# Kernel optimization log

Measured on AMD Instinct MI355X. Metric: run time of the kernel, lower is better.

## Reference

```python
import jax, jax.numpy as jnp
import numpy as np

N = 50000       # nodes
E = 800000      # edges (before self-loops)
IN_DIM = 128
HID = 64
HEADS = 4
C = HID // HEADS  # 16 per-head channels
NEG_SLOPE = 0.2   # PyG GATConv default
BN_EPS = 1e-5


def setup_inputs() -> dict:
    key = jax.random.key(0)
    ks = jax.random.split(key, 16)
    inp = {
        "x": jax.random.normal(ks[0], (N, IN_DIM), jnp.float32),
        "edge_index": jax.random.randint(ks[1], (2, E), 0, N, dtype=jnp.int32),
    }
    def glorot(k, shape):
        fan = sum(shape)
        return jax.random.normal(k, shape, jnp.float32) * jnp.sqrt(2.0 / fan)
    # layer 0: in=IN_DIM, layer 1: in=HID
    inp["W0"] = glorot(ks[2], (IN_DIM, HEADS * C))
    inp["a_src0"] = glorot(ks[3], (HEADS, C))
    inp["a_dst0"] = glorot(ks[4], (HEADS, C))
    inp["b0"] = jnp.zeros((HEADS * C,), jnp.float32)
    inp["g0"] = jnp.ones((HID,), jnp.float32)
    inp["be0"] = jnp.zeros((HID,), jnp.float32)
    inp["W1"] = glorot(ks[5], (HID, HEADS * C))
    inp["a_src1"] = glorot(ks[6], (HEADS, C))
    inp["a_dst1"] = glorot(ks[7], (HEADS, C))
    inp["b1"] = jnp.zeros((HEADS * C,), jnp.float32)
    inp["g1"] = jnp.ones((HID,), jnp.float32)
    inp["be1"] = jnp.zeros((HID,), jnp.float32)
    return inp


def _segment_softmax(e, dst, n):
    # softmax over edges grouped by destination node, per head. e: [Et, H]
    m = jax.ops.segment_max(e, dst, num_segments=n)          # [N, H]
    ex = jnp.exp(e - m[dst])
    s = jax.ops.segment_sum(ex, dst, num_segments=n)         # [N, H]
    return ex / (s[dst] + 1e-16)


def _gat_conv(h, src, dst, W, a_s, a_d, b):
    n = h.shape[0]
    hp = (h @ W).reshape(n, HEADS, C)                        # [N, H, C]
    al_s = jnp.einsum('nhc,hc->nh', hp, a_s)                 # [N, H]
    al_d = jnp.einsum('nhc,hc->nh', hp, a_d)
    e = jax.nn.leaky_relu(al_s[src] + al_d[dst], NEG_SLOPE)  # [Et, H]
    alpha = _segment_softmax(e, dst, n)
    msg = hp[src] * alpha[:, :, None]                        # [Et, H, C]
    out = jax.ops.segment_sum(msg, dst, num_segments=n)      # [N, H, C]
    return out.reshape(n, HEADS * C) + b


def _batch_norm(h, g, b):
    mu = h.mean(axis=0)
    var = h.var(axis=0)
    return (h - mu) * jax.lax.rsqrt(var + BN_EPS) * g + b


def reference(x, edge_index, W0, a_src0, a_dst0, b0, g0, be0,
              W1, a_src1, a_dst1, b1, g1, be1):
    n = x.shape[0]
    loops = jnp.arange(n, dtype=edge_index.dtype)
    src = jnp.concatenate([edge_index[0], loops])  # PyG adds self-loops
    dst = jnp.concatenate([edge_index[1], loops])
    h = _gat_conv(x, src, dst, W0, a_src0, a_dst0, b0)
    h = _batch_norm(h, g0, be0)
    h = jax.nn.relu(h)  # dropout: identity (eval / deterministic)
    h = _gat_conv(h, src, dst, W1, a_src1, a_dst1, b1)
    h = _batch_norm(h, g1, be1)
    return h
```

## Files before the change

kernel.cpp:

```cpp
#include <hip/hip_runtime.h>
#include <hip/hip_fp16.h>

#define CAP 128

template<int K, bool APPLY_BN>
__global__ void __launch_bounds__(256, 4)
gemm_tiled(const float* __restrict__ X, const float* __restrict__ W,
           const float* __restrict__ a_s, const float* __restrict__ a_d,
           const float* __restrict__ bnsum, const float* __restrict__ bnsq,
           const float* __restrict__ g, const float* __restrict__ be,
           __half* __restrict__ hp, float* __restrict__ al_s,
           float* __restrict__ al_d, int n)
{
  __shared__ float Wl[(K / 4) * 64 * 4];
  __shared__ float Xt[64 * K];

  for (int gi = threadIdx.x; gi < (K / 4) * 64; gi += 256) {
    int k4 = gi >> 6, ln = gi & 63;
    float4 w;
    w.x = W[(k4 * 4 + 0) * 64 + ln];
    w.y = W[(k4 * 4 + 1) * 64 + ln];
    w.z = W[(k4 * 4 + 2) * 64 + ln];
    w.w = W[(k4 * 4 + 3) * 64 + ln];
    *(float4*)&Wl[gi * 4] = w;
  }

  int row0 = blockIdx.x * 64;
  int nrows = min(64, n - row0);
  float4 sc, sh;
  if (APPLY_BN) {
    int cg = (threadIdx.x & 15) * 4;
    float inv_n = 1.f / (float)n;
#pragma unroll
    for (int q = 0; q < 4; ++q) {
      float mu  = bnsum[cg + q] * inv_n;
      float var = bnsq[cg + q] * inv_n - mu * mu;
      float s   = g[cg + q] * rsqrtf(var + 1e-5f);
      ((float*)&sc)[q] = s;
      ((float*)&sh)[q] = be[cg + q] - mu * s;
    }
  }
  const float4* src = (const float4*)(X + (size_t)row0 * K);
  int nf4 = nrows * (K / 4);
  for (int i = threadIdx.x; i < nf4; i += 256) {
    float4 v = src[i];
    if (APPLY_BN) {
      v.x = fmaxf(v.x * sc.x + sh.x, 0.f);
      v.y = fmaxf(v.y * sc.y + sh.y, 0.f);
      v.z = fmaxf(v.z * sc.z + sh.z, 0.f);
      v.w = fmaxf(v.w * sc.w + sh.w, 0.f);
    }
    *(float4*)&Xt[i * 4] = v;
  }
  __syncthreads();

  int lane = threadIdx.x & 63;
  int wid  = threadIdx.x >> 6;
  int rbase = wid * 16;
  float acc[16];
#pragma unroll
  for (int r = 0; r < 16; ++r) acc[r] = 0.f;

  for (int k4 = 0; k4 < K / 4; ++k4) {
    float4 wv = *(const float4*)&Wl[(k4 * 64 + lane) * 4];
#pragma unroll
    for (int r = 0; r < 16; ++r) {
      float4 xv = *(const float4*)&Xt[(rbase + r) * K + k4 * 4];
      acc[r] += xv.x * wv.x + xv.y * wv.y + xv.z * wv.z + xv.w * wv.w;
    }
  }

  float as_l = a_s[lane], ad_l = a_d[lane];
  int h = lane >> 4, c = lane & 15;
#pragma unroll
  for (int r = 0; r < 16; ++r) {
    int lr = rbase + r;
    if (lr >= nrows) break;
    int row = row0 + lr;
    float a = acc[r];
    hp[(size_t)row * 64 + lane] = __float2half(a);
    float vs = a * as_l;
    float vd = a * ad_l;
#pragma unroll
    for (int off = 8; off >= 1; off >>= 1) {
      vs += __shfl_xor(vs, off, 64);
      vd += __shfl_xor(vd, off, 64);
    }
    if (c == 0) { al_s[row * 4 + h] = vs; al_d[row * 4 + h] = vd; }
  }
}

__global__ void hist_k(const int* __restrict__ ei, int E, int N, int* __restrict__ count)
{
  int e = blockIdx.x * 256 + threadIdx.x;
  int Et = E + N;
  if (e >= Et) return;
  int d = (e < E) ? ei[E + e] : (e - E);
  atomicAdd(&count[d], 1);
}

__global__ void scan_block_k(const int* __restrict__ count, int* __restrict__ row_ptr,
                             int* __restrict__ partial, int n)
{
  __shared__ int woff[16];
  int tid = threadIdx.x;
  int i = blockIdx.x * 1024 + tid;
  int v = (i < n) ? count[i] : 0;
  int lane = tid & 63, wid = tid >> 6;
  int incl = v;
#pragma unroll
  for (int off = 1; off < 64; off <<= 1) {
    int t = __shfl_up(incl, off, 64);
    if (lane >= off) incl += t;
  }
  if (lane == 63) woff[wid] = incl;
  __syncthreads();
  if (tid < 16) {
    int wv = woff[tid];
    int winc = wv;
#pragma unroll
    for (int off = 1; off < 16; off <<= 1) {
      int t = __shfl_up(winc, off, 64);
      if (tid >= off) winc += t;
    }
    woff[tid] = winc - wv;
    if (tid == 15) partial[blockIdx.x] = winc;
  }
  __syncthreads();
  if (i < n) row_ptr[i] = woff[wid] + incl - v;
}

__global__ void scan_partial_k(int* __restrict__ partial, int* __restrict__ row_ptr,
                               int nb, int n)
{
  int tid = threadIdx.x;
  int v = (tid < nb) ? partial[tid] : 0;
  int incl = v;
#pragma unroll
  for (int off = 1; off < 64; off <<= 1) {
    int t = __shfl_up(incl, off, 64);
    if (tid >= off) incl += t;
  }
  if (tid < nb) partial[tid] = incl - v;
  if (tid == 63) row_ptr[n] = incl;
}

__global__ void scan_add_k(int* __restrict__ row_ptr, int* __restrict__ cursor,
                           const int* __restrict__ partial, int n)
{
  int i = blockIdx.x * 1024 + threadIdx.x;
  if (i < n) {
    int r = row_ptr[i] + partial[blockIdx.x];
    row_ptr[i] = r;
    cursor[i] = r;
  }
}

__global__ void scatter_k(const int* __restrict__ ei, int E, int N,
                          int* __restrict__ cursor, int* __restrict__ col_src)
{
  int e = blockIdx.x * 256 + threadIdx.x;
  int Et = E + N;
  if (e >= Et) return;
  int s, d;
  if (e < E) { s = ei[e]; d = ei[E + e]; } else { s = d = e - E; }
  int pos = atomicAdd(&cursor[d], 1);
  col_src[pos] = s;
}

__global__ void __launch_bounds__(256)
node_agg(const int* __restrict__ row_ptr, const int* __restrict__ col_src,
         const __half* __restrict__ hp, const float* __restrict__ al_s,
         const float* __restrict__ al_d, const float* __restrict__ bias,
         float* __restrict__ hpre, float* __restrict__ bnsum, float* __restrict__ bnsq,
         int n)
{
  __shared__ float sh_ex[4][CAP * 4];
  __shared__ int   sh_s[4][CAP];
  __shared__ float shs[64], shq[64];

  int lane = threadIdx.x & 63;
  int wid  = threadIdx.x >> 6;
  int h    = lane >> 4;
  float b  = bias[lane];
  float lsum = 0.f, lsq = 0.f;
  int nwaves = gridDim.x * 4;

  for (int d = blockIdx.x * 4 + wid; d < n; d += nwaves) {
    int beg = row_ptr[d], end = row_ptr[d + 1];
    int deg = end - beg;
    const float4 ald4 = *(const float4*)(al_d + (size_t)d * 4);
    float outv;

    if (deg <= CAP) {
      float sx = 0.f, sy = 0.f, sz = 0.f, sw = 0.f;
      for (int jb = 0; jb < deg; jb += 64) {
        int jj = jb + lane;
        if (jj < deg) {
          int s = col_src[beg + jj];
          float4 as4 = *(const float4*)(al_s + (size_t)s * 4);
          float ex = as4.x + ald4.x; ex = ex >= 0.f ? ex : 0.2f * ex;
          float ey = as4.y + ald4.y; ey = ey >= 0.f ? ey : 0.2f * ey;
          float ez = as4.z + ald4.z; ez = ez >= 0.f ? ez : 0.2f * ez;
          float ew = as4.w + ald4.w; ew = ew >= 0.f ? ew : 0.2f * ew;
          ex = __expf(ex); ey = __expf(ey); ez = __expf(ez); ew = __expf(ew);
          sh_s[wid][jj] = s;
          *(float4*)&sh_ex[wid][jj * 4] = make_float4(ex, ey, ez, ew);
          sx += ex; sy += ey; sz += ez; sw += ew;
        }
      }
#pragma unroll
      for (int off = 32; off >= 1; off >>= 1) {
        sx += __shfl_xor(sx, off, 64);
        sy += __shfl_xor(sy, off, 64);
        sz += __shfl_xor(sz, off, 64);
        sw += __shfl_xor(sw, off, 64);
      }
      float denom = (h == 0) ? sx : (h == 1) ? sy : (h == 2) ? sz : sw;
      float acc = 0.f;
      int jj = 0;
      for (; jj + 8 <= deg; jj += 8) {
        int s0 = sh_s[wid][jj],     s1 = sh_s[wid][jj + 1];
        int s2 = sh_s[wid][jj + 2], s3 = sh_s[wid][jj + 3];
        int s4 = sh_s[wid][jj + 4], s5 = sh_s[wid][jj + 5];
        int s6 = sh_s[wid][jj + 6], s7 = sh_s[wid][jj + 7];
        float e0 = sh_ex[wid][(jj + 0) * 4 + h], e1 = sh_ex[wid][(jj + 1) * 4 + h];
        float e2 = sh_ex[wid][(jj + 2) * 4 + h], e3 = sh_ex[wid][(jj + 3) * 4 + h];
        float e4 = sh_ex[wid][(jj + 4) * 4 + h], e5 = sh_ex[wid][(jj + 5) * 4 + h];
        float e6 = sh_ex[wid][(jj + 6) * 4 + h], e7 = sh_ex[wid][(jj + 7) * 4 + h];
        acc += e0 * __half2float(hp[(size_t)s0 * 64 + lane]);
        acc += e1 * __half2float(hp[(size_t)s1 * 64 + lane]);
        acc += e2 * __half2float(hp[(size_t)s2 * 64 + lane]);
        acc += e3 * __half2float(hp[(size_t)s3 * 64 + lane]);
        acc += e4 * __half2float(hp[(size_t)s4 * 64 + lane]);
        acc += e5 * __half2float(hp[(size_t)s5 * 64 + lane]);
        acc += e6 * __half2float(hp[(size_t)s6 * 64 + lane]);
        acc += e7 * __half2float(hp[(size_t)s7 * 64 + lane]);
      }
      for (; jj + 4 <= deg; jj += 4) {
        int s0 = sh_s[wid][jj],     s1 = sh_s[wid][jj + 1];
        int s2 = sh_s[wid][jj + 2], s3 = sh_s[wid][jj + 3];
        float e0 = sh_ex[wid][(jj + 0) * 4 + h], e1 = sh_ex[wid][(jj + 1) * 4 + h];
        float e2 = sh_ex[wid][(jj + 2) * 4 + h], e3 = sh_ex[wid][(jj + 3) * 4 + h];
        acc += e0 * __half2float(hp[(size_t)s0 * 64 + lane]);
        acc += e1 * __half2float(hp[(size_t)s1 * 64 + lane]);
        acc += e2 * __half2float(hp[(size_t)s2 * 64 + lane]);
        acc += e3 * __half2float(hp[(size_t)s3 * 64 + lane]);
      }
      for (; jj < deg; ++jj)
        acc += sh_ex[wid][jj * 4 + h] * __half2float(hp[(size_t)sh_s[wid][jj] * 64 + lane]);
      outv = acc / (denom + 1e-16f) + b;
    } else {
      float ald_h = (h == 0) ? ald4.x : (h == 1) ? ald4.y : (h == 2) ? ald4.z : ald4.w;
      float sum = 0.f;
      for (int j = beg; j < end; ++j) {
        int s = col_src[j];
        float v = al_s[s * 4 + h] + ald_h;
        v = (v >= 0.f) ? v : 0.2f * v;
        sum += __expf(v);
      }
      float acc = 0.f;
      for (int j = beg; j < end; ++j) {
        int s = col_src[j];
        float v = al_s[s * 4 + h] + ald_h;
        v = (v >= 0.f) ? v : 0.2f * v;
        acc += __expf(v) * __half2float(hp[(size_t)s * 64 + lane]);
      }
      outv = acc / (sum + 1e-16f) + b;
    }
    hpre[(size_t)d * 64 + lane] = outv;
    lsum += outv; lsq += outv * outv;
  }

  if (threadIdx.x < 64) { shs[threadIdx.x] = 0.f; shq[threadIdx.x] = 0.f; }
  __syncthreads();
  atomicAdd(&shs[lane], lsum);
  atomicAdd(&shq[lane], lsq);
  __syncthreads();
  if (threadIdx.x < 64) {
    atomicAdd(&bnsum[threadIdx.x], shs[threadIdx.x]);
    atomicAdd(&bnsq[threadIdx.x],  shq[threadIdx.x]);
  }
}

__global__ void bn_apply(const float* __restrict__ hpre, const float* __restrict__ bnsum,
                         const float* __restrict__ bnsq, const float* __restrict__ g,
                         const float* __restrict__ be, float* __restrict__ out, int n)
{
  size_t i = (size_t)blockIdx.x * 256 + threadIdx.x;
  size_t total = (size_t)n * 64;
  if (i >= total) return;
  int c = (int)(i & 63);
  float inv_n = 1.f / (float)n;
  float mu  = bnsum[c] * inv_n;
  float var = bnsq[c] * inv_n - mu * mu;
  out[i] = (hpre[i] - mu) * rsqrtf(var + 1e-5f) * g[c] + be[c];
}

extern "C" void kernel_launch(void* const* d_in, const int* in_sizes, int n_in,
                              void* d_out, int out_size, void* d_ws, size_t ws_size,
                              hipStream_t stream) {
  const float* x   = (const float*)d_in[0];
  const int*   ei  = (const int*)d_in[1];
  const float* W0  = (const float*)d_in[2];
  const float* as0 = (const float*)d_in[3];
  const float* ad0 = (const float*)d_in[4];
  const float* b0  = (const float*)d_in[5];
  const float* g0  = (const float*)d_in[6];
  const float* be0 = (const float*)d_in[7];
  const float* W1  = (const float*)d_in[8];
  const float* as1 = (const float*)d_in[9];
  const float* ad1 = (const float*)d_in[10];
  const float* b1  = (const float*)d_in[11];
  const float* g1  = (const float*)d_in[12];
  const float* be1 = (const float*)d_in[13];
  float* out = (float*)d_out;

  int N = in_sizes[0] / 128;
  int E = in_sizes[1] / 2;
  int Et = E + N;

  char* w = (char*)d_ws;
  auto alloc = [&](size_t bytes) {
    char* p = w; w += (bytes + 255) & ~255ull; return p;
  };
  __half* hp    = (__half*)alloc((size_t)N * 64 * 2);
  float*  hpre0 = (float*)alloc((size_t)N * 64 * 4);
  float*  hpre1 = (float*)alloc((size_t)N * 64 * 4);
  float*  als   = (float*)alloc((size_t)N * 4 * 4);
  float*  ald   = (float*)alloc((size_t)N * 4 * 4);
  int*    count = (int*)alloc((size_t)N * 4);
  int*    rowp  = (int*)alloc((size_t)(N + 1) * 4);
  int*    cursor= (int*)alloc((size_t)N * 4);
  int*    parts = (int*)alloc(64 * 4);
  int*    csrc  = (int*)alloc((size_t)Et * 4);
  float*  bnsum = (float*)alloc(64 * 4);
  float*  bnsq  = (float*)alloc(64 * 4);

  dim3 blk(256);
  int gEt   = (Et + 255) / 256;
  int gN64  = (N * 64 + 255) / 256;
  int nb    = (N + 1023) / 1024;
  int gTile = (N + 63) / 64;

  hipMemsetAsync(count, 0, (size_t)N * 4, stream);
  hist_k<<<gEt, blk, 0, stream>>>(ei, E, N, count);
  scan_block_k<<<nb, 1024, 0, stream>>>(count, rowp, parts, N);
  scan_partial_k<<<1, 64, 0, stream>>>(parts, rowp, nb, N);
  scan_add_k<<<nb, 1024, 0, stream>>>(rowp, cursor, parts, N);
  scatter_k<<<gEt, blk, 0, stream>>>(ei, E, N, cursor, csrc);

  hipMemsetAsync(bnsum, 0, 64 * 4, stream);
  hipMemsetAsync(bnsq,  0, 64 * 4, stream);
  gemm_tiled<128, false><<<gTile, blk, 0, stream>>>(x, W0, as0, ad0,
                                                    nullptr, nullptr, nullptr, nullptr,
                                                    hp, als, ald, N);
  node_agg<<<2048, blk, 0, stream>>>(rowp, csrc, hp, als, ald, b0,
                                     hpre0, bnsum, bnsq, N);

  gemm_tiled<64, true><<<gTile, blk, 0, stream>>>(hpre0, W1, as1, ad1,
                                                  bnsum, bnsq, g0, be0,
                                                  hp, als, ald, N);
  hipMemsetAsync(bnsum, 0, 64 * 4, stream);
  hipMemsetAsync(bnsq,  0, 64 * 4, stream);
  node_agg<<<2048, blk, 0, stream>>>(rowp, csrc, hp, als, ald, b1,
                                     hpre1, bnsum, bnsq, N);
  bn_apply<<<gN64, blk, 0, stream>>>(hpre1, bnsum, bnsq, g1, be1, out, N);
}
```

Baseline: 329.7 us.

## Precompute edge attention weights and aggregate two destination nodes per wavefront

Adds a per-edge kernel that computes exp(leaky_relu) attention weights in CSR order, storing them as float4 alongside a new col_dst array. node_agg then reads these precomputed weights and processes two consecutive destination nodes per wavefront, so low-degree nodes use more of the 64 lanes during the gather. It also merges the memsets for the batch-norm accumulators into the count memset and writes the second layer straight into the output buffer. The trade-off is extra global traffic for col_dst and a 16-byte weight per edge, two extra kernel launches, and doubled FMA work in the split accumulation.

```diff
diff --git a/kernel.cpp b/kernel.cpp
--- a/kernel.cpp
+++ b/kernel.cpp
@@ -2,6 +2,10 @@
 #include <hip/hip_fp16.h>
 
 #define CAP 128
+
+__device__ __forceinline__ float sel4(float4 v, int h) {
+  return h == 0 ? v.x : h == 1 ? v.y : h == 2 ? v.z : v.w;
+}
 
 template<int K, bool APPLY_BN>
 __global__ void __launch_bounds__(256, 4)
@@ -157,7 +161,8 @@
 }
 
 __global__ void scatter_k(const int* __restrict__ ei, int E, int N,
-                          int* __restrict__ cursor, int* __restrict__ col_src)
+                          int* __restrict__ cursor, int* __restrict__ col_src,
+                          int* __restrict__ col_dst)
 {
   int e = blockIdx.x * 256 + threadIdx.x;
   int Et = E + N;
@@ -166,17 +171,33 @@
   if (e < E) { s = ei[e]; d = ei[E + e]; } else { s = d = e - E; }
   int pos = atomicAdd(&cursor[d], 1);
   col_src[pos] = s;
+  col_dst[pos] = d;
+}
+
+__global__ void eweight_k(const int* __restrict__ csrc, const int* __restrict__ cdst,
+                          const float* __restrict__ al_s, const float* __restrict__ al_d,
+                          float4* __restrict__ ew, int Et)
+{
+  int e = blockIdx.x * 256 + threadIdx.x;
+  if (e >= Et) return;
+  int s = csrc[e], d = cdst[e];
+  float4 a = *(const float4*)(al_s + (size_t)s * 4);
+  float4 b = *(const float4*)(al_d + (size_t)d * 4);
+  float ex = a.x + b.x; ex = ex >= 0.f ? ex : 0.2f * ex;
+  float ey = a.y + b.y; ey = ey >= 0.f ? ey : 0.2f * ey;
+  float ez = a.z + b.z; ez = ez >= 0.f ? ez : 0.2f * ez;
+  float ewv = a.w + b.w; ewv = ewv >= 0.f ? ewv : 0.2f * ewv;
+  ew[e] = make_float4(__expf(ex), __expf(ey), __expf(ez), __expf(ewv));
 }
 
 __global__ void __launch_bounds__(256)
 node_agg(const int* __restrict__ row_ptr, const int* __restrict__ col_src,
-         const __half* __restrict__ hp, const float* __restrict__ al_s,
-         const float* __restrict__ al_d, const float* __restrict__ bias,
-         float* __restrict__ hpre, float* __restrict__ bnsum, float* __restrict__ bnsq,
-         int n)
-{
-  __shared__ float sh_ex[4][CAP * 4];
+         const float4* __restrict__ ew, const __half* __restrict__ hp,
+         const float* __restrict__ bias, float* __restrict__ hpre,
+         float* __restrict__ bnsum, float* __restrict__ bnsq, int n)
+{
   __shared__ int   sh_s[4][CAP];
+  __shared__ float sh_w[4][CAP * 4];
   __shared__ float shs[64], shq[64];
 
   int lane = threadIdx.x & 63;
@@ -185,91 +206,91 @@
   float b  = bias[lane];
   float lsum = 0.f, lsq = 0.f;
   int nwaves = gridDim.x * 4;
-
-  for (int d = blockIdx.x * 4 + wid; d < n; d += nwaves) {
-    int beg = row_ptr[d], end = row_ptr[d + 1];
-    int deg = end - beg;
-    const float4 ald4 = *(const float4*)(al_d + (size_t)d * 4);
-    float outv;
-
-    if (deg <= CAP) {
-      float sx = 0.f, sy = 0.f, sz = 0.f, sw = 0.f;
-      for (int jb = 0; jb < deg; jb += 64) {
+  int npairs = (n + 1) >> 1;
+
+  for (int p = blockIdx.x * 4 + wid; p < npairs; p += nwaves) {
+    int d = p * 2;
+    bool has1 = (d + 1) < n;
+    int beg0 = row_ptr[d];
+    int end0 = row_ptr[d + 1];
+    int end1 = has1 ? row_ptr[d + 2] : end0;
+    int deg0 = end0 - beg0;
+    int degP = end1 - beg0;
+    float o0, o1 = 0.f;
+
+    if (degP <= CAP) {
+      float p00 = 0.f, p01 = 0.f, p02 = 0.f, p03 = 0.f;
+      float p10 = 0.f, p11 = 0.f, p12 = 0.f, p13 = 0.f;
+      for (int jb = 0; jb < degP; jb += 64) {
         int jj = jb + lane;
-        if (jj < deg) {
-          int s = col_src[beg + jj];
-          float4 as4 = *(const float4*)(al_s + (size_t)s * 4);
-          float ex = as4.x + ald4.x; ex = ex >= 0.f ? ex : 0.2f * ex;
-          float ey = as4.y + ald4.y; ey = ey >= 0.f ? ey : 0.2f * ey;
-          float ez = as4.z + ald4.z; ez = ez >= 0.f ? ez : 0.2f * ez;
-          float ew = as4.w + ald4.w; ew = ew >= 0.f ? ew : 0.2f * ew;
-          ex = __expf(ex); ey = __expf(ey); ez = __expf(ez); ew = __expf(ew);
+        if (jj < degP) {
+          int s = col_src[beg0 + jj];
+          float4 w = ew[beg0 + jj];
           sh_s[wid][jj] = s;
-          *(float4*)&sh_ex[wid][jj * 4] = make_float4(ex, ey, ez, ew);
-          sx += ex; sy += ey; sz += ez; sw += ew;
+          *(float4*)&sh_w[wid][jj * 4] = w;
+          if (jj < deg0) { p00 += w.x; p01 += w.y; p02 += w.z; p03 += w.w; }
+          else           { p10 += w.x; p11 += w.y; p12 += w.z; p13 += w.w; }
         }
       }
 #pragma unroll
       for (int off = 32; off >= 1; off >>= 1) {
-        sx += __shfl_xor(sx, off, 64);
-        sy += __shfl_xor(sy, off, 64);
-        sz += __shfl_xor(sz, off, 64);
-        sw += __shfl_xor(sw, off, 64);
-      }
-      float denom = (h == 0) ? sx : (h == 1) ? sy : (h == 2) ? sz : sw;
-      float acc = 0.f;
-      int jj = 0;
-      for (; jj + 8 <= deg; jj += 8) {
-        int s0 = sh_s[wid][jj],     s1 = sh_s[wid][jj + 1];
-        int s2 = sh_s[wid][jj + 2], s3 = sh_s[wid][jj + 3];
-        int s4 = sh_s[wid][jj + 4], s5 = sh_s[wid][jj + 5];
-        int s6 = sh_s[wid][jj + 6], s7 = sh_s[wid][jj + 7];
-        float e0 = sh_ex[wid][(jj + 0) * 4 + h], e1 = sh_ex[wid][(jj + 1) * 4 + h];
-        float e2 = sh_ex[wid][(jj + 2) * 4 + h], e3 = sh_ex[wid][(jj + 3) * 4 + h];
-        float e4 = sh_ex[wid][(jj + 4) * 4 + h], e5 = sh_ex[wid][(jj + 5) * 4 + h];
-        float e6 = sh_ex[wid][(jj + 6) * 4 + h], e7 = sh_ex[wid][(jj + 7) * 4 + h];
-        acc += e0 * __half2float(hp[(size_t)s0 * 64 + lane]);
-        acc += e1 * __half2float(hp[(size_t)s1 * 64 + lane]);
-        acc += e2 * __half2float(hp[(size_t)s2 * 64 + lane]);
-        acc += e3 * __half2float(hp[(size_t)s3 * 64 + lane]);
-        acc += e4 * __half2float(hp[(size_t)s4 * 64 + lane]);
-        acc += e5 * __half2float(hp[(size_t)s5 * 64 + lane]);
-        acc += e6 * __half2float(hp[(size_t)s6 * 64 + lane]);
-        acc += e7 * __half2float(hp[(size_t)s7 * 64 + lane]);
-      }
-      for (; jj + 4 <= deg; jj += 4) {
-        int s0 = sh_s[wid][jj],     s1 = sh_s[wid][jj + 1];
-        int s2 = sh_s[wid][jj + 2], s3 = sh_s[wid][jj + 3];
-        float e0 = sh_ex[wid][(jj + 0) * 4 + h], e1 = sh_ex[wid][(jj + 1) * 4 + h];
-        float e2 = sh_ex[wid][(jj + 2) * 4 + h], e3 = sh_ex[wid][(jj + 3) * 4 + h];
-        acc += e0 * __half2float(hp[(size_t)s0 * 64 + lane]);
-        acc += e1 * __half2float(hp[(size_t)s1 * 64 + lane]);
-        acc += e2 * __half2float(hp[(size_t)s2 * 64 + lane]);
-        acc += e3 * __half2float(hp[(size_t)s3 * 64 + lane]);
-      }
-      for (; jj < deg; ++jj)
-        acc += sh_ex[wid][jj * 4 + h] * __half2float(hp[(size_t)sh_s[wid][jj] * 64 + lane]);
-      outv = acc / (denom + 1e-16f) + b;
+        p00 += __shfl_xor(p00, off, 64); p01 += __shfl_xor(p01, off, 64);
+        p02 += __shfl_xor(p02, off, 64); p03 += __shfl_xor(p03, off, 64);
+        p10 += __shfl_xor(p10, off, 64); p11 += __shfl_xor(p11, off, 64);
+        p12 += __shfl_xor(p12, off, 64); p13 += __shfl_xor(p13, off, 64);
+      }
+      float den0 = (h == 0) ? p00 : (h == 1) ? p01 : (h == 2) ? p02 : p03;
+      float den1 = (h == 0) ? p10 : (h == 1) ? p11 : (h == 2) ? p12 : p13;
+
+      float acc0 = 0.f, acc1 = 0.f;
+      int j = 0;
+      for (; j + 8 <= degP; j += 8) {
+#pragma unroll
+        for (int k = 0; k < 8; ++k) {
+          int jk = j + k;
+          int s = sh_s[wid][jk];
+          float wh = sh_w[wid][jk * 4 + h];
+          float v = __half2float(hp[(size_t)s * 64 + lane]);
+          float w0 = (jk < deg0) ? wh : 0.f;
+          acc0 += w0 * v;
+          acc1 += (wh - w0) * v;
+        }
+      }
+      for (; j < degP; ++j) {
+        int s = sh_s[wid][j];
+        float wh = sh_w[wid][j * 4 + h];
+        float v = __half2float(hp[(size_t)s * 64 + lane]);
+        float w0 = (j < deg0) ? wh : 0.f;
+        acc0 += w0 * v;
+        acc1 += (wh - w0) * v;
+      }
+      o0 = acc0 / (den0 + 1e-16f) + b;
+      if (has1) o1 = acc1 / (den1 + 1e-16f) + b;
     } else {
-      float ald_h = (h == 0) ? ald4.x : (h == 1) ? ald4.y : (h == 2) ? ald4.z : ald4.w;
-      float sum = 0.f;
-      for (int j = beg; j < end; ++j) {
-        int s = col_src[j];
-        float v = al_s[s * 4 + h] + ald_h;
-        v = (v >= 0.f) ? v : 0.2f * v;
-        sum += __expf(v);
-      }
-      float acc = 0.f;
-      for (int j = beg; j < end; ++j) {
-        int s = col_src[j];
-        float v = al_s[s * 4 + h] + ald_h;
-        v = (v >= 0.f) ? v : 0.2f * v;
-        acc += __expf(v) * __half2float(hp[(size_t)s * 64 + lane]);
-      }
-      outv = acc / (sum + 1e-16f) + b;
-    }
-    hpre[(size_t)d * 64 + lane] = outv;
-    lsum += outv; lsq += outv * outv;
+      float den = 0.f, acc = 0.f;
+      for (int j = beg0; j < end0; ++j) {
+        float wh = sel4(ew[j], h);
+        den += wh;
+        acc += wh * __half2float(hp[(size_t)col_src[j] * 64 + lane]);
+      }
+      o0 = acc / (den + 1e-16f) + b;
+      if (has1) {
+        den = 0.f; acc = 0.f;
+        for (int j = end0; j < end1; ++j) {
+          float wh = sel4(ew[j], h);
+          den += wh;
+          acc += wh * __half2float(hp[(size_t)col_src[j] * 64 + lane]);
+        }
+        o1 = acc / (den + 1e-16f) + b;
+      }
+    }
+
+    hpre[(size_t)d * 64 + lane] = o0;
+    lsum += o0; lsq += o0 * o0;
+    if (has1) {
+      hpre[(size_t)(d + 1) * 64 + lane] = o1;
+      lsum += o1; lsq += o1 * o1;
+    }
   }
 
   if (threadIdx.x < 64) { shs[threadIdx.x] = 0.f; shq[threadIdx.x] = 0.f; }
@@ -283,9 +304,9 @@
   }
 }
 
-__global__ void bn_apply(const float* __restrict__ hpre, const float* __restrict__ bnsum,
+__global__ void bn_apply(float* __restrict__ buf, const float* __restrict__ bnsum,
                          const float* __restrict__ bnsq, const float* __restrict__ g,
-                         const float* __restrict__ be, float* __restrict__ out, int n)
+                         const float* __restrict__ be, int n)
 {
   size_t i = (size_t)blockIdx.x * 256 + threadIdx.x;
   size_t total = (size_t)n * 64;
@@ -294,7 +315,7 @@
   float inv_n = 1.f / (float)n;
   float mu  = bnsum[c] * inv_n;
   float var = bnsq[c] * inv_n - mu * mu;
-  out[i] = (hpre[i] - mu) * rsqrtf(var + 1e-5f) * g[c] + be[c];
+  buf[i] = (buf[i] - mu) * rsqrtf(var + 1e-5f) * g[c] + be[c];
 }
 
 extern "C" void kernel_launch(void* const* d_in, const int* in_sizes, int n_in,
@@ -324,18 +345,21 @@
   auto alloc = [&](size_t bytes) {
     char* p = w; w += (bytes + 255) & ~255ull; return p;
   };
+  int*    count = (int*)alloc((size_t)N * 4 + 4 * 64 * 4);
+  float*  bnsum0 = (float*)(count + N);
+  float*  bnsq0  = bnsum0 + 64;
+  float*  bnsum1 = bnsq0 + 64;
+  float*  bnsq1  = bnsum1 + 64;
   __half* hp    = (__half*)alloc((size_t)N * 64 * 2);
   float*  hpre0 = (float*)alloc((size_t)N * 64 * 4);
-  float*  hpre1 = (float*)alloc((size_t)N * 64 * 4);
   float*  als   = (float*)alloc((size_t)N * 4 * 4);
   float*  ald   = (float*)alloc((size_t)N * 4 * 4);
-  int*    count = (int*)alloc((size_t)N * 4);
   int*    rowp  = (int*)alloc((size_t)(N + 1) * 4);
   int*    cursor= (int*)alloc((size_t)N * 4);
   int*    parts = (int*)alloc(64 * 4);
   int*    csrc  = (int*)alloc((size_t)Et * 4);
-  float*  bnsum = (float*)alloc(64 * 4);
-  float*  bnsq  = (float*)alloc(64 * 4);
+  int*    cdst  = (int*)alloc((size_t)Et * 4);
+  float4* ew    = (float4*)alloc((size_t)Et * 16);
 
   dim3 blk(256);
   int gEt   = (Et + 255) / 256;
@@ -343,27 +367,26 @@
   int nb    = (N + 1023) / 1024;
   int gTile = (N + 63) / 64;
 
-  hipMemsetAsync(count, 0, (size_t)N * 4, stream);
+  hipMemsetAsync(count, 0, (size_t)N * 4 + 4 * 64 * 4, stream);
+
   hist_k<<<gEt, blk, 0, stream>>>(ei, E, N, count);
   scan_block_k<<<nb, 1024, 0, stream>>>(count, rowp, parts, N);
   scan_partial_k<<<1, 64, 0, stream>>>(parts, rowp, nb, N);
   scan_add_k<<<nb, 1024, 0, stream>>>(rowp, cursor, parts, N);
-  scatter_k<<<gEt, blk, 0, stream>>>(ei, E, N, cursor, csrc);
-
-  hipMemsetAsync(bnsum, 0, 64 * 4, stream);
-  hipMemsetAsync(bnsq,  0, 64 * 4, stream);
+  scatter_k<<<gEt, blk, 0, stream>>>(ei, E, N, cursor, csrc, cdst);
+
   gemm_tiled<128, false><<<gTile, blk, 0, stream>>>(x, W0, as0, ad0,
                                                     nullptr, nullptr, nullptr, nullptr,
                                                     hp, als, ald, N);
-  node_agg<<<2048, blk, 0, stream>>>(rowp, csrc, hp, als, ald, b0,
-                                     hpre0, bnsum, bnsq, N);
+  eweight_k<<<gEt, blk, 0, stream>>>(csrc, cdst, als, ald, ew, Et);
+  node_agg<<<2048, blk, 0, stream>>>(rowp, csrc, ew, hp, b0,
+                                     hpre0, bnsum0, bnsq0, N);
 
   gemm_tiled<64, true><<<gTile, blk, 0, stream>>>(hpre0, W1, as1, ad1,
-                                                  bnsum, bnsq, g0, be0,
+                                                  bnsum0, bnsq0, g0, be0,
                                                   hp, als, ald, N);
-  hipMemsetAsync(bnsum, 0, 64 * 4, stream);
-  hipMemsetAsync(bnsq,  0, 64 * 4, stream);
-  node_agg<<<2048, blk, 0, stream>>>(rowp, csrc, hp, als, ald, b1,
-                                     hpre1, bnsum, bnsq, N);
-  bn_apply<<<gN64, blk, 0, stream>>>(hpre1, bnsum, bnsq, g1, be1, out, N);
-}
+  eweight_k<<<gEt, blk, 0, stream>>>(csrc, cdst, als, ald, ew, Et);
+  node_agg<<<2048, blk, 0, stream>>>(rowp, csrc, ew, hp, b1,
+                                     out, bnsum1, bnsq1, N);
+  bn_apply<<<gN64, blk, 0, stream>>>(out, bnsum1, bnsq1, g1, be1, N);
+}
```

Result: no change. 331.4 us (+0.5%).
